# Optimization experiments

Hardware: AMD Instinct MI355X
Metric: run time of the kernel (lower is better)

## Reference

```python
import jax, jax.numpy as jnp
import numpy as np

B, C, G = 8, 64, 65536
IN_DIM, OUT_DIM = 64, 64
SLOPE = 0.1


def setup_inputs() -> dict:
    key = jax.random.key(0)
    ks = jax.random.split(key, 5)
    features = jax.random.normal(ks[0], (B, C, G), dtype=jnp.float32)
    # Conv2d(in*2, out, 1, bias=False) weights, squeezed to [out, in*2]
    W0 = jax.random.normal(ks[1], (OUT_DIM, IN_DIM * 2), dtype=jnp.float32) * (1.0 / np.sqrt(IN_DIM * 2))
    W1 = jax.random.normal(ks[2], (OUT_DIM, OUT_DIM * 2), dtype=jnp.float32) * (1.0 / np.sqrt(OUT_DIM * 2))
    W2 = jax.random.normal(ks[3], (OUT_DIM, OUT_DIM * 2), dtype=jnp.float32) * (1.0 / np.sqrt(OUT_DIM * 2))
    W3 = jax.random.normal(ks[4], (OUT_DIM, OUT_DIM * 2), dtype=jnp.float32) * (1.0 / np.sqrt(OUT_DIM * 2))
    return {"features": features, "W0": W0, "W1": W1, "W2": W2, "W3": W3}


def _layer(x, W):
    # x: [B, C, G]; tile the first group's features and build (x, x - x0)
    x0 = x[:, :, :1]                               # [B, C, 1]
    h = jnp.concatenate([x, x - x0], axis=1)       # [B, 2C, G]
    # 1x1 conv == pointwise linear over channels
    y = jnp.einsum("oc,bcg->bog", W, h)            # [B, O, G]
    return jax.nn.leaky_relu(y, negative_slope=SLOPE)


def reference(features, W0, W1, W2, W3):
    x = features
    for W in (W0, W1, W2, W3):
        x = _layer(x, W)
    return jnp.max(x, axis=-1)                     # [B, O]
```

## Files before the change

kernel.cpp:

```cpp
#include <hip/hip_runtime.h>


#define G_TOT 65536

typedef _Float16 hf2 __attribute__((ext_vector_type(2)));
typedef _Float16 hf4 __attribute__((ext_vector_type(4)));
typedef _Float16 hf8 __attribute__((ext_vector_type(8)));
typedef float float4_ __attribute__((ext_vector_type(4)));

static __device__ __forceinline__ hf2 pkh(float x, float y) {
    return __builtin_bit_cast(hf2, __builtin_amdgcn_cvt_pkrtz(x, y));
}


__global__ __launch_bounds__(512) void ge_prep(
    const float* __restrict__ feat,
    const float* __restrict__ W0, const float* __restrict__ W1,
    const float* __restrict__ W2, const float* __restrict__ W3,
    float* __restrict__ ws)
{
    const int tid = threadIdx.x;
    unsigned* maxenc = (unsigned*)(ws + 18432);
    maxenc[tid] = 0u;

    for (int i = tid; i < 4 * 64 * 64; i += 512) {
        int l = i >> 12, o = (i >> 6) & 63, c = i & 63;
        const float* Wl = (l == 0) ? W0 : (l == 1) ? W1 : (l == 2) ? W2 : W3;
        ws[i] = Wl[o * 128 + c] + Wl[o * 128 + 64 + c];
    }

    __shared__ float lw[64][129];
    __shared__ float xA[8][64];
    __shared__ float xB[8][64];
    const int b = tid >> 6, o = tid & 63;
    xA[b][o] = feat[(size_t)(b * 64 + o) * G_TOT];

    float* nbias = ws + 16384;
    for (int l = 0; l < 4; ++l) {
        const float* Wl = (l == 0) ? W0 : (l == 1) ? W1 : (l == 2) ? W2 : W3;
        for (int i = tid; i < 64 * 128; i += 512) lw[i >> 7][i & 127] = Wl[i];
        __syncthreads();
        const float* src = (l & 1) ? &xB[0][0] : &xA[0][0];
        float*       dst = (l & 1) ? &xA[0][0] : &xB[0][0];
        float s1 = 0.f, s2 = 0.f;
        for (int c = 0; c < 64; ++c) {
            float xv = src[b * 64 + c];
            s1 += lw[o][c] * xv;
            s2 += lw[o][64 + c] * xv;
        }
        nbias[b * 256 + l * 64 + o] = -s2;
        dst[b * 64 + o] = fmaxf(s1, 0.1f * s1);
        __syncthreads();
    }
}

__global__ __launch_bounds__(256, 2) void ge_main(
    const float* __restrict__ feat,
    const float* __restrict__ ws_wa,
    const float* __restrict__ nbias,
    unsigned* __restrict__ maxenc)
{
    __shared__ _Float16 lws[16384];
    __shared__ float lbias[256];
    __shared__ float blockmax[4][64];
    const int tid = threadIdx.x;
    const int b = blockIdx.x >> 7;

    for (int gi = tid; gi < 4096; gi += 256) {
        int hi = gi & 1, ln = (gi >> 1) & 63, f = gi >> 7;
        int pr = f & 1, mt = (f >> 1) & 3, l = f >> 3;
        int o = (mt << 4) + (ln & 15);
        int c = (((pr << 1) + hi) << 4) + ((ln >> 4) << 2);
        float4_ wv = *(const float4_*)&ws_wa[((l << 6) + o) * 64 + c];
        union { hf2 h2[2]; hf4 h4; } u;
        u.h2[0] = pkh(wv[0], wv[1]);
        u.h2[1] = pkh(wv[2], wv[3]);
        *(hf4*)&lws[gi << 2] = u.h4;
    }
    lbias[tid] = nbias[(b << 8) + tid];
    __syncthreads();

    const int w = tid >> 6, lane = tid & 63, q = lane >> 4, n = lane & 15;
    const int g0 = ((blockIdx.x & 127) << 9) + (w << 7);
    const float* Xrow = feat + (size_t)b * 64 * G_TOT + (size_t)(q << 2) * G_TOT;
    const hf4 k01 = { (_Float16)0.1f, (_Float16)0.1f, (_Float16)0.1f, (_Float16)0.1f };

    float rmax[4][4];
#pragma unroll
    for (int mt = 0; mt < 4; ++mt)
#pragma unroll
        for (int j = 0; j < 4; ++j) rmax[mt][j] = -__builtin_inff();

    float cur[16];
    {
        int gcol = g0 + n;
#pragma unroll
        for (int kf = 0; kf < 4; ++kf)
#pragma unroll
            for (int r = 0; r < 4; ++r)
                cur[kf * 4 + r] = Xrow[(size_t)((kf << 4) + r) * G_TOT + gcol];
    }

#pragma unroll 1
    for (int nt = 0; nt < 8; ++nt) {
        float nxt[16];
        {
            int gcol = g0 + (((nt + 1) & 7) << 4) + n;
#pragma unroll
            for (int kf = 0; kf < 4; ++kf)
#pragma unroll
                for (int r = 0; r < 4; ++r)
                    nxt[kf * 4 + r] = Xrow[(size_t)((kf << 4) + r) * G_TOT + gcol];
        }

        hf4 bf[4];
#pragma unroll
        for (int kf = 0; kf < 4; ++kf) {
            union { hf2 h2[2]; hf4 h4; } u;
            u.h2[0] = pkh(cur[kf * 4 + 0], cur[kf * 4 + 1]);
            u.h2[1] = pkh(cur[kf * 4 + 2], cur[kf * 4 + 3]);
            bf[kf] = u.h4;
        }

#pragma unroll
        for (int l = 0; l < 4; ++l) {
            float4_ acc[4];
#pragma unroll
            for (int mt = 0; mt < 4; ++mt)
                acc[mt] = *(const float4_*)&lbias[(l << 6) + (mt << 4) + (q << 2)];
#pragma unroll
            for (int mt = 0; mt < 4; ++mt) {
#pragma unroll
                for (int pr = 0; pr < 2; ++pr) {
                    union { hf8 h8; hf4 h4[2]; } ua;
                    ua.h8 = *(const hf8*)&lws[((((((l << 2) + mt) << 1) + pr) << 6) + lane) << 3];
                    acc[mt] = __builtin_amdgcn_mfma_f32_16x16x16f16(ua.h4[0], bf[(pr << 1) + 0], acc[mt], 0, 0, 0);
                    acc[mt] = __builtin_amdgcn_mfma_f32_16x16x16f16(ua.h4[1], bf[(pr << 1) + 1], acc[mt], 0, 0, 0);
                }
            }
            if (l < 3) {
#pragma unroll
                for (int mt = 0; mt < 4; ++mt) {
                    union { hf2 h2[2]; hf4 h4; } u;
                    u.h2[0] = pkh(acc[mt][0], acc[mt][1]);
                    u.h2[1] = pkh(acc[mt][2], acc[mt][3]);
                    hf4 h = u.h4;
                    h = __builtin_elementwise_max(h, h * k01);
                    bf[mt] = h;
                }
            } else {
#pragma unroll
                for (int mt = 0; mt < 4; ++mt)
#pragma unroll
                    for (int j = 0; j < 4; ++j) {
                        float y = acc[mt][j];
                        rmax[mt][j] = fmaxf(rmax[mt][j], fmaxf(y, 0.1f * y));
                    }
            }
        }
#pragma unroll
        for (int i = 0; i < 16; ++i) cur[i] = nxt[i];
    }

#pragma unroll
    for (int mt = 0; mt < 4; ++mt)
#pragma unroll
        for (int j = 0; j < 4; ++j) {
            float v = rmax[mt][j];
            v = fmaxf(v, __shfl_xor(v, 1, 64));
            v = fmaxf(v, __shfl_xor(v, 2, 64));
            v = fmaxf(v, __shfl_xor(v, 4, 64));
            v = fmaxf(v, __shfl_xor(v, 8, 64));
            rmax[mt][j] = v;
        }
    if (n == 0) {
#pragma unroll
        for (int mt = 0; mt < 4; ++mt)
#pragma unroll
            for (int j = 0; j < 4; ++j)
                blockmax[w][(mt << 4) + (q << 2) + j] = rmax[mt][j];
    }
    __syncthreads();
    if (tid < 64) {
        float v = fmaxf(fmaxf(blockmax[0][tid], blockmax[1][tid]),
                        fmaxf(blockmax[2][tid], blockmax[3][tid]));
        unsigned s = __float_as_uint(v);
        unsigned enc = (s & 0x80000000u) ? ~s : (s | 0x80000000u);
        atomicMax(&maxenc[b * 64 + tid], enc);
    }
}

__global__ void ge_final(const unsigned* __restrict__ maxenc, float* __restrict__ out)
{
    int i = threadIdx.x;
    if (i < 512) {
        unsigned u = maxenc[i];
        unsigned s = (u & 0x80000000u) ? (u ^ 0x80000000u) : ~u;
        out[i] = __uint_as_float(s);
    }
}

extern "C" void kernel_launch(void* const* d_in, const int* in_sizes, int n_in,
                              void* d_out, int out_size, void* d_ws, size_t ws_size,
                              hipStream_t stream) {
    const float* feat = (const float*)d_in[0];
    const float* W0 = (const float*)d_in[1];
    const float* W1 = (const float*)d_in[2];
    const float* W2 = (const float*)d_in[3];
    const float* W3 = (const float*)d_in[4];
    float* ws = (float*)d_ws;
    unsigned* maxenc = (unsigned*)(ws + 18432);

    ge_prep<<<1, 512, 0, stream>>>(feat, W0, W1, W2, W3, ws);
    ge_main<<<1024, 256, 0, stream>>>(feat, ws, ws + 16384, maxenc);
    ge_final<<<1, 512, 0, stream>>>(maxenc, (float*)d_out);
}
```

Measured before the change: 229.2 us.

## Split prep across blocks and widen main kernel to 512 threads per block

The prep kernel now runs nine blocks: one per batch computes the x0 bias chain, and a separate block sums the weights and zeroes the max buffer, so the serial single-block prologue gets shorter. The main kernel doubles its block size to 8 waves, each covering 64 columns in 4 iterations instead of 128 in 8. This is meant to raise occupancy and shorten the per-wave serial loop so memory latency is hidden better. In exchange each block's weight staging in LDS is amortised over less work per wave, and the higher occupancy target may pressure registers.

```diff
diff --git a/kernel.cpp b/kernel.cpp
--- a/kernel.cpp
+++ b/kernel.cpp
@@ -13,48 +13,52 @@
 }
 
 
-__global__ __launch_bounds__(512) void ge_prep(
+__global__ __launch_bounds__(256) void ge_prep(
     const float* __restrict__ feat,
     const float* __restrict__ W0, const float* __restrict__ W1,
     const float* __restrict__ W2, const float* __restrict__ W3,
     float* __restrict__ ws)
 {
     const int tid = threadIdx.x;
-    unsigned* maxenc = (unsigned*)(ws + 18432);
-    maxenc[tid] = 0u;
-
-    for (int i = tid; i < 4 * 64 * 64; i += 512) {
-        int l = i >> 12, o = (i >> 6) & 63, c = i & 63;
-        const float* Wl = (l == 0) ? W0 : (l == 1) ? W1 : (l == 2) ? W2 : W3;
-        ws[i] = Wl[o * 128 + c] + Wl[o * 128 + 64 + c];
-    }
-
+    const int blk = blockIdx.x;
     __shared__ float lw[64][129];
-    __shared__ float xA[8][64];
-    __shared__ float xB[8][64];
-    const int b = tid >> 6, o = tid & 63;
-    xA[b][o] = feat[(size_t)(b * 64 + o) * G_TOT];
-
+    __shared__ float x0[2][64];
+
+    if (blk == 8) {
+        unsigned* maxenc = (unsigned*)(ws + 18432);
+        maxenc[tid] = 0u; maxenc[tid + 256] = 0u;
+        for (int i = tid; i < 4 * 64 * 64; i += 256) {
+            int l = i >> 12, o = (i >> 6) & 63, c = i & 63;
+            const float* Wl = (l == 0) ? W0 : (l == 1) ? W1 : (l == 2) ? W2 : W3;
+            ws[i] = Wl[o * 128 + c] + Wl[o * 128 + 64 + c];
+        }
+        return;
+    }
+
+    const int b = blk;
+    if (tid < 64) x0[0][tid] = feat[(size_t)(b * 64 + tid) * G_TOT];
     float* nbias = ws + 16384;
     for (int l = 0; l < 4; ++l) {
         const float* Wl = (l == 0) ? W0 : (l == 1) ? W1 : (l == 2) ? W2 : W3;
-        for (int i = tid; i < 64 * 128; i += 512) lw[i >> 7][i & 127] = Wl[i];
+        for (int i = tid; i < 64 * 128; i += 256) lw[i >> 7][i & 127] = Wl[i];
         __syncthreads();
-        const float* src = (l & 1) ? &xB[0][0] : &xA[0][0];
-        float*       dst = (l & 1) ? &xA[0][0] : &xB[0][0];
-        float s1 = 0.f, s2 = 0.f;
-        for (int c = 0; c < 64; ++c) {
-            float xv = src[b * 64 + c];
-            s1 += lw[o][c] * xv;
-            s2 += lw[o][64 + c] * xv;
-        }
-        nbias[b * 256 + l * 64 + o] = -s2;
-        dst[b * 64 + o] = fmaxf(s1, 0.1f * s1);
+        if (tid < 64) {
+            const int o = tid;
+            const float* src = x0[l & 1];
+            float s1 = 0.f, s2 = 0.f;
+            for (int c = 0; c < 64; ++c) {
+                float xv = src[c];
+                s1 += lw[o][c] * xv;
+                s2 += lw[o][64 + c] * xv;
+            }
+            nbias[b * 256 + l * 64 + o] = -s2;
+            x0[(l & 1) ^ 1][o] = fmaxf(s1, 0.1f * s1);
+        }
         __syncthreads();
     }
 }
 
-__global__ __launch_bounds__(256, 2) void ge_main(
+__global__ __launch_bounds__(512, 8) void ge_main(
     const float* __restrict__ feat,
     const float* __restrict__ ws_wa,
     const float* __restrict__ nbias,
@@ -62,11 +66,11 @@
 {
     __shared__ _Float16 lws[16384];
     __shared__ float lbias[256];
-    __shared__ float blockmax[4][64];
+    __shared__ float blockmax[8][64];
     const int tid = threadIdx.x;
     const int b = blockIdx.x >> 7;
 
-    for (int gi = tid; gi < 4096; gi += 256) {
+    for (int gi = tid; gi < 4096; gi += 512) {
         int hi = gi & 1, ln = (gi >> 1) & 63, f = gi >> 7;
         int pr = f & 1, mt = (f >> 1) & 3, l = f >> 3;
         int o = (mt << 4) + (ln & 15);
@@ -77,11 +81,11 @@
         u.h2[1] = pkh(wv[2], wv[3]);
         *(hf4*)&lws[gi << 2] = u.h4;
     }
-    lbias[tid] = nbias[(b << 8) + tid];
+    if (tid < 256) lbias[tid] = nbias[(b << 8) + tid];
     __syncthreads();
 
     const int w = tid >> 6, lane = tid & 63, q = lane >> 4, n = lane & 15;
-    const int g0 = ((blockIdx.x & 127) << 9) + (w << 7);
+    const int g0 = ((blockIdx.x & 127) << 9) + (w << 6);
     const float* Xrow = feat + (size_t)b * 64 * G_TOT + (size_t)(q << 2) * G_TOT;
     const hf4 k01 = { (_Float16)0.1f, (_Float16)0.1f, (_Float16)0.1f, (_Float16)0.1f };
 
@@ -102,10 +106,10 @@
     }
 
 #pragma unroll 1
-    for (int nt = 0; nt < 8; ++nt) {
+    for (int nt = 0; nt < 4; ++nt) {
         float nxt[16];
         {
-            int gcol = g0 + (((nt + 1) & 7) << 4) + n;
+            int gcol = g0 + (((nt + 1) & 3) << 4) + n;
 #pragma unroll
             for (int kf = 0; kf < 4; ++kf)
 #pragma unroll
@@ -182,8 +186,9 @@
     }
     __syncthreads();
     if (tid < 64) {
-        float v = fmaxf(fmaxf(blockmax[0][tid], blockmax[1][tid]),
-                        fmaxf(blockmax[2][tid], blockmax[3][tid]));
+        float v = blockmax[0][tid];
+#pragma unroll
+        for (int ww = 1; ww < 8; ++ww) v = fmaxf(v, blockmax[ww][tid]);
         unsigned s = __float_as_uint(v);
         unsigned enc = (s & 0x80000000u) ? ~s : (s | 0x80000000u);
         atomicMax(&maxenc[b * 64 + tid], enc);
@@ -211,7 +216,7 @@
     float* ws = (float*)d_ws;
     unsigned* maxenc = (unsigned*)(ws + 18432);
 
-    ge_prep<<<1, 512, 0, stream>>>(feat, W0, W1, W2, W3, ws);
-    ge_main<<<1024, 256, 0, stream>>>(feat, ws, ws + 16384, maxenc);
+    ge_prep<<<9, 256, 0, stream>>>(feat, W0, W1, W2, W3, ws);
+    ge_main<<<1024, 512, 0, stream>>>(feat, ws, ws + 16384, maxenc);
     ge_final<<<1, 512, 0, stream>>>(maxenc, (float*)d_out);
 }
```

New measurement: 547.0 us. 139% more time.
